# Optimization experiments

Measured on AMD Instinct MI355X. Metric: run time of the kernel, lower is better.

The kernel has to match this reference:

```python
import jax, jax.numpy as jnp
import numpy as np

K = 5           # kernel_size
STRIDE = 1
DILATION = 1
PAD = 2         # padding='same': total = dilation*(K-1) = 4, left = 2, right = 2 (reflect mode)


def setup_inputs() -> dict:
    key = jax.random.key(0)
    k1, k2, k3, k4 = jax.random.split(key, 4)
    B, C_in, C_out, L = 8, 64, 64, 16384
    x = jax.random.normal(k1, (B, C_in, L), dtype=jnp.float32)
    # offsets broadcast over channels: (B, 1, L_out, K); L_out == L for padding='same'
    offsets = jax.random.normal(k2, (B, 1, L, K), dtype=jnp.float32)
    weight = jax.random.normal(k3, (C_out, C_in, K), dtype=jnp.float32) * (1.0 / np.sqrt(C_in * K))
    bias = jax.random.normal(k4, (C_out,), dtype=jnp.float32) * 0.05
    return {"x": x, "offsets": offsets, "weight": weight, "bias": bias}


def _deform_interp(xp, offsets):
    # xp: (B, C, Lp) padded input; offsets: (B, 1, Lo, K)
    B, C, Lp = xp.shape
    Lo, Kk = offsets.shape[-2], offsets.shape[-1]
    t0 = (STRIDE * jnp.arange(Lo, dtype=xp.dtype))[:, None]          # base sample positions
    dil = (DILATION * jnp.arange(Kk, dtype=xp.dtype))[None, :]       # dilated kernel positions
    T = jnp.clip(t0 + dil + offsets, 0.0, float(Lp - 1))             # (B, 1, Lo, K)
    i0 = jnp.clip(jnp.floor(T).astype(jnp.int32), 0, Lp - 2)
    frac = T - i0.astype(xp.dtype)                                   # linear-interp weight
    i0b = jnp.broadcast_to(i0, (B, C, Lo, Kk)).reshape(B, C, Lo * Kk)
    g0 = jnp.take_along_axis(xp, i0b, axis=-1).reshape(B, C, Lo, Kk)
    g1 = jnp.take_along_axis(xp, i0b + 1, axis=-1).reshape(B, C, Lo, Kk)
    return g0 * (1.0 - frac) + g1 * frac                             # (B, C, Lo, K)


def reference(x, offsets, weight, bias):
    # 'same' padding with reflect mode
    xp = jnp.pad(x, ((0, 0), (0, 0), (PAD, PAD)), mode="reflect")
    v = _deform_interp(xp, offsets)                                  # (B, C, Lo, K)
    # flatten(-2,-1) + conv1d(stride=K, groups=1) == contraction over (c, k) per output pos
    out = jnp.einsum("bclk,ock->bol", v, weight) + bias[None, :, None]
    return out
```

## Files before the change

kernel.cpp:

```cpp
#include <hip/hip_runtime.h>

#define BATCH 8
#define CIN   64
#define COUT  64
#define LEN   16384
#define KS    5
#define PADW  2
#define LP    (LEN + 2*PADW)
#define TTB   128
#define XROWS 104
#define XM    14

typedef __attribute__((ext_vector_type(8)))  short short8;
typedef __attribute__((ext_vector_type(4)))  float f32x4;

__device__ __forceinline__ unsigned short bf16r(float f) {
    unsigned u = __builtin_bit_cast(unsigned, f);
    u += 0x7FFF + ((u >> 16) & 1);
    return (unsigned short)(u >> 16);
}
__device__ __forceinline__ unsigned fpack(float a, float b) {
    unsigned ua = __builtin_bit_cast(unsigned, a) + 0x8000u;
    unsigned ub = __builtin_bit_cast(unsigned, b) + 0x8000u;
    return __builtin_amdgcn_perm(ub, ua, 0x07060302);
}
__device__ __forceinline__ int reflmap(int s) {
    return (s < PADW) ? (PADW - s) : ((s < LEN + PADW) ? (s - PADW) : (2*LEN - s));
}

__global__ void wfrag_kernel(const float* __restrict__ w, unsigned short* __restrict__ wf) {
    int el = blockIdx.x * 256 + threadIdx.x;
    int e    = el & 7;
    int lane = (el >> 3) & 63;
    int kk   = (el >> 9) % 10;
    int ot   = el / 5120;
    int o    = ot * 16 + (lane & 15);
    int kg   = kk * 32 + ((lane >> 4) << 3) + e;
    int ktap = kg >> 6;
    int c    = kg & 63;
    wf[el] = bf16r(w[(o * 64 + c) * 5 + ktap]);
}

__global__ __launch_bounds__(256, 4) void deform_mfma_kernel(
    const float* __restrict__ x, const float* __restrict__ offs,
    const unsigned short* __restrict__ wf, const float* __restrict__ bias,
    float* __restrict__ out)
{
    __shared__ __align__(16) unsigned short xtl[2][XROWS * 64];

    const int tid = threadIdx.x;
    const int bid = blockIdx.x;
    const int bt  = (bid & 7) * 128 + (bid >> 3);
    const int b   = bt >> 7;
    const int T0  = (bt & 127) * TTB;
    const int w   = tid >> 6;
    const int lane = tid & 63;
    const int pl  = lane & 15;
    const int s   = lane >> 4;

    const float* xb0 = x + (size_t)b * CIN * LEN;
    const unsigned short* wfl = wf + (size_t)lane * 8;

    float of0[KS], of1[KS];
    {
        const int tcா = T0 + w * 16 + pl;
        #pragma unroll
        for (int k = 0; k < KS; ++k) of0[k] = offs[((size_t)(b * LEN + tcா)) * KS + k];
        #pragma unroll
        for (int k = 0; k < KS; ++k) of1[k] = offs[((size_t)(b * LEN + tcா + 64)) * KS + k];
    }

    float4 vA0[2], vA1[2], vB0[2], vB1[2];
    int stg_fast;

#define STAGE_LOAD(t0s)                                                        \
    stg_fast = ((t0s) >= 16 && (t0s) + 88 <= LEN);                             \
    if (stg_fast) {                                                            \
        const float* src0 = xb0 + ((t0s) - 16);                                \
        _Pragma("unroll")                                                      \
        for (int rep = 0; rep < 2; ++rep) {                                    \
            int task = rep * 256 + tid;            \
            if (task < 416) {                                                  \
                int c2 = task / 13, q = task - c2 * 13;                        \
                const float* p0 = src0 + (size_t)(2 * c2) * LEN + 8 * q;       \
                vA0[rep] = *(const float4*)p0;                                 \
                vA1[rep] = *(const float4*)(p0 + 4);                           \
                vB0[rep] = *(const float4*)(p0 + LEN);                         \
                vB1[rep] = *(const float4*)(p0 + LEN + 4);                     \
            }                                                                  \
        }                                                                      \
    }

#define STAGE_WRITE(dst, t0s)                                                  \
    if (stg_fast) {                                                            \
        _Pragma("unroll")                                                      \
        for (int rep = 0; rep < 2; ++rep) {                                    \
            int task = rep * 256 + tid;                                        \
            if (task < 416) {                                                  \
                int c2 = task / 13, q = task - c2 * 13;                        \
                float av[8] = {vA0[rep].x, vA0[rep].y, vA0[rep].z, vA0[rep].w, \
                               vA1[rep].x, vA1[rep].y, vA1[rep].z, vA1[rep].w};\
                float bv[8] = {vB0[rep].x, vB0[rep].y, vB0[rep].z, vB0[rep].w, \
                               vB1[rep].x, vB1[rep].y, vB1[rep].z, vB1[rep].w};\
                _Pragma("unroll")                                              \
                for (int i = 0; i < 8; ++i) {                                  \
                    int r = 8 * q + i;                                         \
                    *(unsigned*)((char*)(dst) + r * 128 +                      \
                        ((4 * c2) ^ ((r & 7) << 4))) = fpack(av[i], bv[i]);    \
                }                                                              \
            }                                                                  \
        }                                                                      \
    } else {                                                                   \
        const int S0e = (t0s) - XM;                                            \
        _Pragma("unroll")                                                      \
        for (int rep = 0; rep < 26; ++rep) {                                   \
            int idx = rep * 256 + tid;                    \
            int r = idx >> 6, c = idx & 63;                                    \
            int sp = min(max(S0e + r, 0), LP - 1);                             \
            *(unsigned short*)((char*)(dst) + r * 128 +                        \
                ((2 * c) ^ ((r & 7) << 4))) = bf16r(xb0[(size_t)c * LEN + reflmap(sp)]); \
        }                                                                      \
    }

#define LERPW(dst, w0, w1, f)                                                  \
    {                                                                          \
        float g0a = __builtin_bit_cast(float, (w0) << 16);                     \
        float g1a = __builtin_bit_cast(float, (w1) << 16);                     \
        float g0b = __builtin_bit_cast(float, (w0) & 0xFFFF0000u);             \
        float g1b = __builtin_bit_cast(float, (w1) & 0xFFFF0000u);             \
        dst = fpack(fmaf(f, g1a - g0a, g0a), fmaf(f, g1b - g0b, g0b));         \
    }

#define GATHF(pw, XB, R0A, FRA, k, mm)                                         \
    {                                                                          \
        const int r0 = R0A[k], r1 = r0 + 1;                                    \
        const float f = FRA[k];                                                \
        uint4 u0 = *(const uint4*)((const char*)(XB) + r0 * 128 + ((mm) ^ ((r0 & 7) << 4))); \
        uint4 u1 = *(const uint4*)((const char*)(XB) + r1 * 128 + ((mm) ^ ((r1 & 7) << 4))); \
        LERPW(pw.x, u0.x, u1.x, f) LERPW(pw.y, u0.y, u1.y, f)                  \
        LERPW(pw.z, u0.z, u1.z, f) LERPW(pw.w, u0.w, u1.w, f)                  \
    }

#define GATHS(pw, I0A, FRA, k, m)                                              \
    {                                                                          \
        const float f = FRA[k];                                                \
        int j0 = reflmap(I0A[k]), j1 = reflmap(I0A[k] + 1);                    \
        const float* xc = xb0 + (size_t)((m) << 3) * LEN;                      \
        unsigned pv[4];                                                        \
        _Pragma("unroll")                                                      \
        for (int e = 0; e < 4; ++e) {                                          \
            float ga0 = xc[j0], ga1 = xc[j1];                                  \
            float lo = fmaf(f, ga1 - ga0, ga0);                                \
            float gb0 = xc[LEN + j0], gb1 = xc[LEN + j1];                      \
            float hi = fmaf(f, gb1 - gb0, gb0);                                \
            pv[e] = fpack(lo, hi);                                             \
            xc += 2 * LEN;                                                     \
        }                                                                      \
        pw = uint4{pv[0], pv[1], pv[2], pv[3]};                                \
    }

#define MFMA8(kk, pw0, pw1)                                                    \
    {                                                                          \
        short8 bv0 = __builtin_bit_cast(short8, pw0);                          \
        short8 bv1 = __builtin_bit_cast(short8, pw1);                          \
        short8 a0 = *(const short8*)&wfl[(0 * 10 + (kk)) * 512];               \
        short8 a1 = *(const short8*)&wfl[(1 * 10 + (kk)) * 512];               \
        short8 a2 = *(const short8*)&wfl[(2 * 10 + (kk)) * 512];               \
        short8 a3 = *(const short8*)&wfl[(3 * 10 + (kk)) * 512];               \
        accA0 = __builtin_amdgcn_mfma_f32_16x16x32_bf16(a0, bv0, accA0, 0, 0, 0); \
        accB0 = __builtin_amdgcn_mfma_f32_16x16x32_bf16(a0, bv1, accB0, 0, 0, 0); \
        accA1 = __builtin_amdgcn_mfma_f32_16x16x32_bf16(a1, bv0, accA1, 0, 0, 0); \
        accB1 = __builtin_amdgcn_mfma_f32_16x16x32_bf16(a1, bv1, accB1, 0, 0, 0); \
        accA2 = __builtin_amdgcn_mfma_f32_16x16x32_bf16(a2, bv0, accA2, 0, 0, 0); \
        accB2 = __builtin_amdgcn_mfma_f32_16x16x32_bf16(a2, bv1, accB2, 0, 0, 0); \
        accA3 = __builtin_amdgcn_mfma_f32_16x16x32_bf16(a3, bv0, accA3, 0, 0, 0); \
        accB3 = __builtin_amdgcn_mfma_f32_16x16x32_bf16(a3, bv1, accB3, 0, 0, 0); \
    }

#define FUSED(kk)                                                              \
    {                                                                          \
        const int k  = (kk) >> 1;                                              \
        const int mm = ((((kk) & 1) << 2) + s) * 16;                           \
        uint4 pw0, pw1;                                                        \
        GATHF(pw0, xtl[0], r00, fr0, k, mm)                                    \
        GATHF(pw1, xtl[1], r01, fr1, k, mm)                                    \
        MFMA8(kk, pw0, pw1)                                                    \
    }

#define CHECKED1(kk, pw, R0A, I0A, FRA, XB)                                    \
    {                                                                          \
        const int k = (kk) >> 1;                                               \
        const int m = (((kk) & 1) << 2) + s;                                   \
        if ((unsigned)R0A[k] <= (unsigned)(XROWS - 2)) {                       \
            GATHF(pw, XB, R0A, FRA, k, m * 16)                                 \
        } else {                                                               \
            GATHS(pw, I0A, FRA, k, m)                                          \
        }                                                                      \
    }

#define FUSEDC(kk)                                                             \
    {                                                                          \
        uint4 pw0, pw1;                                                        \
        CHECKED1(kk, pw0, r00, i00, fr0, xtl[0])                               \
        CHECKED1(kk, pw1, r01, i01, fr1, xtl[1])                               \
        MFMA8(kk, pw0, pw1)                                                    \
    }

    STAGE_LOAD(T0);
    STAGE_WRITE(xtl[0], T0);
    STAGE_LOAD(T0 + 64);

    int i00[KS], i01[KS], r00[KS], r01[KS];
    float fr0[KS], fr1[KS];
    bool fastg = true;
    {
        const int tc0 = T0 + w * 16 + pl;
        #pragma unroll
        for (int k = 0; k < KS; ++k) {
            float T = (float)(tc0 + k) + of0[k];
            T = fminf(fmaxf(T, 0.0f), (float)(LP - 1));
            int i0 = (int)floorf(T);
            i0 = min(i0, LP - 2); i0 = max(i0, 0);
            i00[k] = i0; fr0[k] = T - (float)i0; r00[k] = i0 - (T0 - XM);
            fastg = fastg && ((unsigned)r00[k] <= (unsigned)(XROWS - 2));
        }
        #pragma unroll
        for (int k = 0; k < KS; ++k) {
            float T = (float)(tc0 + 64 + k) + of1[k];
            T = fminf(fmaxf(T, 0.0f), (float)(LP - 1));
            int i0 = (int)floorf(T);
            i0 = min(i0, LP - 2); i0 = max(i0, 0);
            i01[k] = i0; fr1[k] = T - (float)i0; r01[k] = i0 - (T0 + 64 - XM);
            fastg = fastg && ((unsigned)r01[k] <= (unsigned)(XROWS - 2));
        }
    }

    STAGE_WRITE(xtl[1], T0 + 64);
    __syncthreads();

    f32x4 accA0 = {}, accA1 = {}, accA2 = {}, accA3 = {};
    f32x4 accB0 = {}, accB1 = {}, accB2 = {}, accB3 = {};
    if (fastg) {
        FUSED(0) FUSED(1) FUSED(2) FUSED(3) FUSED(4)
        FUSED(5) FUSED(6) FUSED(7) FUSED(8) FUSED(9)
    } else {
        FUSEDC(0) FUSEDC(1) FUSEDC(2) FUSEDC(3) FUSEDC(4)
        FUSEDC(5) FUSEDC(6) FUSEDC(7) FUSEDC(8) FUSEDC(9)
    }

    {
        const int tc0 = T0 + w * 16 + pl;
        #pragma unroll
        for (int ot = 0; ot < 4; ++ot) {
            const f32x4 aA = (ot==0)?accA0:(ot==1)?accA1:(ot==2)?accA2:accA3;
            const f32x4 aB = (ot==0)?accB0:(ot==1)?accB1:(ot==2)?accB2:accB3;
            #pragma unroll
            for (int r = 0; r < 4; ++r) {
                int o = ot * 16 + s * 4 + r;
                float bvv = bias[o];
                float* op = out + ((size_t)(b * COUT + o)) * LEN + tc0;
                op[0]  = aA[r] + bvv;
                op[64] = aB[r] + bvv;
            }
        }
    }
#undef FUSEDC
#undef CHECKED1
#undef FUSED
#undef MFMA8
#undef GATHS
#undef GATHF
#undef LERPW
#undef STAGE_WRITE
#undef STAGE_LOAD
}

extern "C" void kernel_launch(void* const* d_in, const int* in_sizes, int n_in,
                              void* d_out, int out_size, void* d_ws, size_t ws_size,
                              hipStream_t stream) {
    const float* x    = (const float*)d_in[0];
    const float* offs = (const float*)d_in[1];
    const float* w    = (const float*)d_in[2];
    const float* bias = (const float*)d_in[3];
    float* out = (float*)d_out;
    unsigned short* wf = (unsigned short*)d_ws;

    wfrag_kernel<<<80, 256, 0, stream>>>(w, wf);
    deform_mfma_kernel<<<BATCH * (LEN / TTB), 256, 0, stream>>>(x, offs, wf, bias, out);
}
```

Measured before the change: 31.83 us.

## Use 256-position tiles with 512 threads, shared x tile and weights in LDS

Doubles the per-block output tile to 256 positions with 512 threads and stages a single shared bf16 x tile of 296 rows, replacing the two separate 104-row halo tiles. The pre-fragmented weights are also copied into LDS once per block instead of being read from global memory per MFMA step. This reduces redundant halo loading and repeated global weight reads, but LDS use rises to about 78 KB per block, which limits occupancy. The earlier software pipelining of the two stage loads is also dropped.

```diff
diff --git a/kernel.cpp b/kernel.cpp
--- a/kernel.cpp
+++ b/kernel.cpp
@@ -7,8 +7,8 @@
 #define KS    5
 #define PADW  2
 #define LP    (LEN + 2*PADW)
-#define TTB   128
-#define XROWS 104
+#define TTB   256
+#define XROWS 296
 #define XM    14
 
 typedef __attribute__((ext_vector_type(8)))  short short8;
@@ -41,86 +41,97 @@
     wf[el] = bf16r(w[(o * 64 + c) * 5 + ktap]);
 }
 
-__global__ __launch_bounds__(256, 4) void deform_mfma_kernel(
+__global__ __launch_bounds__(512, 4) void deform_mfma_kernel(
     const float* __restrict__ x, const float* __restrict__ offs,
-    const unsigned short* __restrict__ wf, const float* __restrict__ bias,
+    const unsigned short* __restrict__ wfg, const float* __restrict__ bias,
     float* __restrict__ out)
 {
-    __shared__ __align__(16) unsigned short xtl[2][XROWS * 64];
+    __shared__ __align__(16) unsigned short wfl_lds[20480];
+    __shared__ __align__(16) unsigned short xt[XROWS * 64];
 
     const int tid = threadIdx.x;
     const int bid = blockIdx.x;
-    const int bt  = (bid & 7) * 128 + (bid >> 3);
-    const int b   = bt >> 7;
-    const int T0  = (bt & 127) * TTB;
+    const int bt  = (bid & 7) * 64 + (bid >> 3);
+    const int b   = bt >> 6;
+    const int T0  = (bt & 63) * TTB;
     const int w   = tid >> 6;
     const int lane = tid & 63;
     const int pl  = lane & 15;
     const int s   = lane >> 4;
+    const int S0  = T0 - XM;
 
     const float* xb0 = x + (size_t)b * CIN * LEN;
-    const unsigned short* wfl = wf + (size_t)lane * 8;
-
+
+    {
+        const uint4* srcw = (const uint4*)wfg;
+        uint4* dstw = (uint4*)wfl_lds;
+        #pragma unroll
+        for (int rep = 0; rep < 5; ++rep)
+            dstw[rep * 512 + tid] = srcw[rep * 512 + tid];
+    }
+
+    const int tc0 = T0 + w * 16 + pl;
     float of0[KS], of1[KS];
-    {
-        const int tcா = T0 + w * 16 + pl;
-        #pragma unroll
-        for (int k = 0; k < KS; ++k) of0[k] = offs[((size_t)(b * LEN + tcா)) * KS + k];
-        #pragma unroll
-        for (int k = 0; k < KS; ++k) of1[k] = offs[((size_t)(b * LEN + tcா + 64)) * KS + k];
-    }
-
-    float4 vA0[2], vA1[2], vB0[2], vB1[2];
-    int stg_fast;
-
-#define STAGE_LOAD(t0s)                                                        \
-    stg_fast = ((t0s) >= 16 && (t0s) + 88 <= LEN);                             \
-    if (stg_fast) {                                                            \
-        const float* src0 = xb0 + ((t0s) - 16);                                \
-        _Pragma("unroll")                                                      \
-        for (int rep = 0; rep < 2; ++rep) {                                    \
-            int task = rep * 256 + tid;            \
-            if (task < 416) {                                                  \
-                int c2 = task / 13, q = task - c2 * 13;                        \
-                const float* p0 = src0 + (size_t)(2 * c2) * LEN + 8 * q;       \
-                vA0[rep] = *(const float4*)p0;                                 \
-                vA1[rep] = *(const float4*)(p0 + 4);                           \
-                vB0[rep] = *(const float4*)(p0 + LEN);                         \
-                vB1[rep] = *(const float4*)(p0 + LEN + 4);                     \
-            }                                                                  \
-        }                                                                      \
-    }
-
-#define STAGE_WRITE(dst, t0s)                                                  \
-    if (stg_fast) {                                                            \
-        _Pragma("unroll")                                                      \
-        for (int rep = 0; rep < 2; ++rep) {                                    \
-            int task = rep * 256 + tid;                                        \
-            if (task < 416) {                                                  \
-                int c2 = task / 13, q = task - c2 * 13;                        \
-                float av[8] = {vA0[rep].x, vA0[rep].y, vA0[rep].z, vA0[rep].w, \
-                               vA1[rep].x, vA1[rep].y, vA1[rep].z, vA1[rep].w};\
-                float bv[8] = {vB0[rep].x, vB0[rep].y, vB0[rep].z, vB0[rep].w, \
-                               vB1[rep].x, vB1[rep].y, vB1[rep].z, vB1[rep].w};\
-                _Pragma("unroll")                                              \
-                for (int i = 0; i < 8; ++i) {                                  \
-                    int r = 8 * q + i;                                         \
-                    *(unsigned*)((char*)(dst) + r * 128 +                      \
-                        ((4 * c2) ^ ((r & 7) << 4))) = fpack(av[i], bv[i]);    \
-                }                                                              \
-            }                                                                  \
-        }                                                                      \
-    } else {                                                                   \
-        const int S0e = (t0s) - XM;                                            \
-        _Pragma("unroll")                                                      \
-        for (int rep = 0; rep < 26; ++rep) {                                   \
-            int idx = rep * 256 + tid;                    \
-            int r = idx >> 6, c = idx & 63;                                    \
-            int sp = min(max(S0e + r, 0), LP - 1);                             \
-            *(unsigned short*)((char*)(dst) + r * 128 +                        \
-                ((2 * c) ^ ((r & 7) << 4))) = bf16r(xb0[(size_t)c * LEN + reflmap(sp)]); \
-        }                                                                      \
-    }
+    #pragma unroll
+    for (int k = 0; k < KS; ++k) {
+        of0[k] = offs[((size_t)(b * LEN + tc0)) * KS + k];
+        of1[k] = offs[((size_t)(b * LEN + tc0 + 128)) * KS + k];
+    }
+
+    if (T0 >= 16 && T0 <= LEN - 280) {
+        const float* src0 = xb0 + (T0 - 16);
+        #pragma unroll
+        for (int rep = 0; rep < 3; ++rep) {
+            int task = rep * 512 + tid;
+            if (task < 1184) {
+                int c2 = task / 37, q = task - c2 * 37;
+                const float* p0 = src0 + (size_t)(2 * c2) * LEN + 8 * q;
+                float4 a0 = *(const float4*)p0;
+                float4 a1 = *(const float4*)(p0 + 4);
+                float4 b0 = *(const float4*)(p0 + LEN);
+                float4 b1 = *(const float4*)(p0 + LEN + 4);
+                float av[8] = {a0.x, a0.y, a0.z, a0.w, a1.x, a1.y, a1.z, a1.w};
+                float bv[8] = {b0.x, b0.y, b0.z, b0.w, b1.x, b1.y, b1.z, b1.w};
+                #pragma unroll
+                for (int i = 0; i < 8; ++i) {
+                    int r = 8 * q + i;
+                    *(unsigned*)((char*)xt + r * 128 +
+                        ((4 * c2) ^ ((r & 7) << 4))) = fpack(av[i], bv[i]);
+                }
+            }
+        }
+    } else {
+        #pragma unroll
+        for (int rep = 0; rep < 37; ++rep) {
+            int idx = rep * 512 + tid;
+            int r = idx >> 6, c = idx & 63;
+            int sp = min(max(S0 + r, 0), LP - 1);
+            *(unsigned short*)((char*)xt + r * 128 +
+                ((2 * c) ^ ((r & 7) << 4))) = bf16r(xb0[(size_t)c * LEN + reflmap(sp)]);
+        }
+    }
+
+    int i00[KS], i01[KS], r00[KS], r01[KS];
+    float fr0[KS], fr1[KS];
+    bool fastg = true;
+    #pragma unroll
+    for (int k = 0; k < KS; ++k) {
+        float T = (float)(tc0 + k) + of0[k];
+        T = fminf(fmaxf(T, 0.0f), (float)(LP - 1));
+        int i0 = (int)floorf(T);
+        i0 = min(i0, LP - 2); i0 = max(i0, 0);
+        i00[k] = i0; fr0[k] = T - (float)i0; r00[k] = i0 - S0;
+        fastg = fastg && ((unsigned)r00[k] <= (unsigned)(XROWS - 2));
+        float T1 = (float)(tc0 + 128 + k) + of1[k];
+        T1 = fminf(fmaxf(T1, 0.0f), (float)(LP - 1));
+        int i1 = (int)floorf(T1);
+        i1 = min(i1, LP - 2); i1 = max(i1, 0);
+        i01[k] = i1; fr1[k] = T1 - (float)i1; r01[k] = i1 - S0;
+        fastg = fastg && ((unsigned)r01[k] <= (unsigned)(XROWS - 2));
+    }
+    __syncthreads();
+
+    const unsigned short* wfl = wfl_lds + (size_t)lane * 8;
 
 #define LERPW(dst, w0, w1, f)                                                  \
     {                                                                          \
@@ -131,12 +142,12 @@
         dst = fpack(fmaf(f, g1a - g0a, g0a), fmaf(f, g1b - g0b, g0b));         \
     }
 
-#define GATHF(pw, XB, R0A, FRA, k, mm)                                         \
+#define GATHF(pw, R0A, FRA, k, mm)                                             \
     {                                                                          \
         const int r0 = R0A[k], r1 = r0 + 1;                                    \
         const float f = FRA[k];                                                \
-        uint4 u0 = *(const uint4*)((const char*)(XB) + r0 * 128 + ((mm) ^ ((r0 & 7) << 4))); \
-        uint4 u1 = *(const uint4*)((const char*)(XB) + r1 * 128 + ((mm) ^ ((r1 & 7) << 4))); \
+        uint4 u0 = *(const uint4*)((const char*)xt + r0 * 128 + ((mm) ^ ((r0 & 7) << 4))); \
+        uint4 u1 = *(const uint4*)((const char*)xt + r1 * 128 + ((mm) ^ ((r1 & 7) << 4))); \
         LERPW(pw.x, u0.x, u1.x, f) LERPW(pw.y, u0.y, u1.y, f)                  \
         LERPW(pw.z, u0.z, u1.z, f) LERPW(pw.w, u0.w, u1.w, f)                  \
     }
@@ -182,17 +193,17 @@
         const int k  = (kk) >> 1;                                              \
         const int mm = ((((kk) & 1) << 2) + s) * 16;                           \
         uint4 pw0, pw1;                                                        \
-        GATHF(pw0, xtl[0], r00, fr0, k, mm)                                    \
-        GATHF(pw1, xtl[1], r01, fr1, k, mm)                                    \
+        GATHF(pw0, r00, fr0, k, mm)                                            \
+        GATHF(pw1, r01, fr1, k, mm)                                            \
         MFMA8(kk, pw0, pw1)                                                    \
     }
 
-#define CHECKED1(kk, pw, R0A, I0A, FRA, XB)                                    \
+#define CHECKED1(kk, pw, R0A, I0A, FRA)                                        \
     {                                                                          \
         const int k = (kk) >> 1;                                               \
         const int m = (((kk) & 1) << 2) + s;                                   \
         if ((unsigned)R0A[k] <= (unsigned)(XROWS - 2)) {                       \
-            GATHF(pw, XB, R0A, FRA, k, m * 16)                                 \
+            GATHF(pw, R0A, FRA, k, m * 16)                                     \
         } else {                                                               \
             GATHS(pw, I0A, FRA, k, m)                                          \
         }                                                                      \
@@ -201,42 +212,10 @@
 #define FUSEDC(kk)                                                             \
     {                                                                          \
         uint4 pw0, pw1;                                                        \
-        CHECKED1(kk, pw0, r00, i00, fr0, xtl[0])                               \
-        CHECKED1(kk, pw1, r01, i01, fr1, xtl[1])                               \
+        CHECKED1(kk, pw0, r00, i00, fr0)                                       \
+        CHECKED1(kk, pw1, r01, i01, fr1)                                       \
         MFMA8(kk, pw0, pw1)                                                    \
     }
-
-    STAGE_LOAD(T0);
-    STAGE_WRITE(xtl[0], T0);
-    STAGE_LOAD(T0 + 64);
-
-    int i00[KS], i01[KS], r00[KS], r01[KS];
-    float fr0[KS], fr1[KS];
-    bool fastg = true;
-    {
-        const int tc0 = T0 + w * 16 + pl;
-        #pragma unroll
-        for (int k = 0; k < KS; ++k) {
-            float T = (float)(tc0 + k) + of0[k];
-            T = fminf(fmaxf(T, 0.0f), (float)(LP - 1));
-            int i0 = (int)floorf(T);
-            i0 = min(i0, LP - 2); i0 = max(i0, 0);
-            i00[k] = i0; fr0[k] = T - (float)i0; r00[k] = i0 - (T0 - XM);
-            fastg = fastg && ((unsigned)r00[k] <= (unsigned)(XROWS - 2));
-        }
-        #pragma unroll
-        for (int k = 0; k < KS; ++k) {
-            float T = (float)(tc0 + 64 + k) + of1[k];
-            T = fminf(fmaxf(T, 0.0f), (float)(LP - 1));
-            int i0 = (int)floorf(T);
-            i0 = min(i0, LP - 2); i0 = max(i0, 0);
-            i01[k] = i0; fr1[k] = T - (float)i0; r01[k] = i0 - (T0 + 64 - XM);
-            fastg = fastg && ((unsigned)r01[k] <= (unsigned)(XROWS - 2));
-        }
-    }
-
-    STAGE_WRITE(xtl[1], T0 + 64);
-    __syncthreads();
 
     f32x4 accA0 = {}, accA1 = {}, accA2 = {}, accA3 = {};
     f32x4 accB0 = {}, accB1 = {}, accB2 = {}, accB3 = {};
@@ -248,20 +227,17 @@
         FUSEDC(5) FUSEDC(6) FUSEDC(7) FUSEDC(8) FUSEDC(9)
     }
 
-    {
-        const int tc0 = T0 + w * 16 + pl;
-        #pragma unroll
-        for (int ot = 0; ot < 4; ++ot) {
-            const f32x4 aA = (ot==0)?accA0:(ot==1)?accA1:(ot==2)?accA2:accA3;
-            const f32x4 aB = (ot==0)?accB0:(ot==1)?accB1:(ot==2)?accB2:accB3;
-            #pragma unroll
-            for (int r = 0; r < 4; ++r) {
-                int o = ot * 16 + s * 4 + r;
-                float bvv = bias[o];
-                float* op = out + ((size_t)(b * COUT + o)) * LEN + tc0;
-                op[0]  = aA[r] + bvv;
-                op[64] = aB[r] + bvv;
-            }
+    #pragma unroll
+    for (int ot = 0; ot < 4; ++ot) {
+        const f32x4 aA = (ot==0)?accA0:(ot==1)?accA1:(ot==2)?accA2:accA3;
+        const f32x4 aB = (ot==0)?accB0:(ot==1)?accB1:(ot==2)?accB2:accB3;
+        #pragma unroll
+        for (int r = 0; r < 4; ++r) {
+            int o = ot * 16 + s * 4 + r;
+            float bvv = bias[o];
+            float* op = out + ((size_t)(b * COUT + o)) * LEN + tc0;
+            op[0]   = aA[r] + bvv;
+            op[128] = aB[r] + bvv;
         }
     }
 #undef FUSEDC
@@ -271,8 +247,6 @@
 #undef GATHS
 #undef GATHF
 #undef LERPW
-#undef STAGE_WRITE
-#undef STAGE_LOAD
 }
 
 extern "C" void kernel_launch(void* const* d_in, const int* in_sizes, int n_in,
@@ -286,5 +260,5 @@
     unsigned short* wf = (unsigned short*)d_ws;
 
     wfrag_kernel<<<80, 256, 0, stream>>>(w, wf);
-    deform_mfma_kernel<<<BATCH * (LEN / TTB), 256, 0, stream>>>(x, offs, wf, bias, out);
-}
+    deform_mfma_kernel<<<BATCH * (LEN / TTB), 512, 0, stream>>>(x, offs, wf, bias, out);
+}
```

Result: slower. 34.22 us (+7.5%).
